# Optimization experiments

Measured on AMD Instinct MI355X. Metric: run time of the kernel, lower is better.

Reference implementation:

```python
import jax, jax.numpy as jnp
import numpy as np

DIM, HEADS = 1024, 16
HEAD_DIM = DIM // HEADS
SCALE = HEAD_DIM ** -0.5


def setup_inputs() -> dict:
    key = jax.random.key(0)
    ks = jax.random.split(key, 5)
    B, N = 2, 2048
    x = jax.random.normal(ks[0], (B, N, DIM), dtype=jnp.float32)
    freqs = jax.random.normal(ks[1], (N, HEAD_DIM // 2), dtype=jnp.float32)
    w_qkv = jax.random.normal(ks[2], (3 * DIM, DIM), dtype=jnp.float32) * 0.02
    w_proj = jax.random.normal(ks[3], (DIM, DIM), dtype=jnp.float32) * 0.02
    b_proj = jnp.zeros((DIM,), dtype=jnp.float32)
    return {"x": x, "freqs": freqs, "w_qkv": w_qkv, "w_proj": w_proj, "b_proj": b_proj}


def _apply_rotary(t, cos, sin):
    # t: (B,N,H,D); cos/sin: (1,N,1,D//2)
    B, N, H, D = t.shape
    tp = t.reshape(B, N, H, D // 2, 2)
    x1, x2 = tp[..., 0], tp[..., 1]
    out = jnp.stack([x1 * cos - x2 * sin, x1 * sin + x2 * cos], axis=-1)
    return out.reshape(B, N, H, D)


def reference(x, freqs, w_qkv, w_proj, b_proj):
    B, N, C = x.shape
    H, D = HEADS, HEAD_DIM
    qkv = (x @ w_qkv.T).reshape(B, N, 3, H, D)  # fused QKV projection
    q, k, v = qkv[:, :, 0], qkv[:, :, 1], qkv[:, :, 2]  # each (B,N,H,D)
    cos = jnp.cos(freqs)[None, :, None, :]  # (1,N,1,D/2)
    sin = jnp.sin(freqs)[None, :, None, :]
    q = _apply_rotary(q, cos, sin)
    k = _apply_rotary(k, cos, sin)
    # SDPA: scores (B,H,N,N)
    scores = jnp.einsum("bqhd,bkhd->bhqk", q, k) * SCALE
    attn = jax.nn.softmax(scores, axis=-1)
    out = jnp.einsum("bhqk,bkhd->bqhd", attn, v).reshape(B, N, C)
    return out @ w_proj.T + b_proj
```

## Files before the change

kernel.cpp:

```cpp
#include <hip/hip_runtime.h>
#include <hip/hip_bf16.h>
#include <stdint.h>

#define BATCH   2
#define SEQ     2048
#define CDIM    1024
#define NHEAD   16
#define HDIM    64
#define MROWS   (BATCH*SEQ)
#define QKVN    (3*CDIM)
#define ATT_SCALE 0.125f

typedef __hip_bfloat16 bf16;
using bf16x8 = __attribute__((ext_vector_type(8))) __bf16;
using f32x4  = __attribute__((ext_vector_type(4))) float;

__device__ __forceinline__ void gld16(const void* g, void* l) {
    __builtin_amdgcn_global_load_lds(
        (__attribute__((address_space(1))) void*)(void*)(g),
        (__attribute__((address_space(3))) void*)(l),
        16, 0, 0);
}

__device__ __forceinline__ f32x4 mfma16x16x32(bf16x8 a, bf16x8 b, f32x4 c) {
    return __builtin_amdgcn_mfma_f32_16x16x32_bf16(a, b, c, 0, 0, 0);
}

__device__ __forceinline__ void store_out(bf16* p, float v) { *p = __float2bfloat16(v); }
__device__ __forceinline__ void store_out(float* p, float v) { *p = v; }

__global__ __launch_bounds__(256)
void cvt_kernel(const float* __restrict__ x, const float* __restrict__ wq,
                const float* __restrict__ wp, bf16* __restrict__ xb,
                bf16* __restrict__ wqb, bf16* __restrict__ wpb) {
    const size_t NX = (size_t)MROWS*CDIM/4;
    const size_t NQ = (size_t)QKVN*CDIM/4;
    size_t i4 = (size_t)blockIdx.x*256 + threadIdx.x;
    const float* src; bf16* dst; size_t off;
    if (i4 < NX)           { src = x;  dst = xb;  off = i4; }
    else if (i4 < NX + NQ) { src = wq; dst = wqb; off = i4 - NX; }
    else                   { src = wp; dst = wpb; off = i4 - NX - NQ; }
    float4 v = ((const float4*)src)[off];
    bf16 o[4] = { __float2bfloat16(v.x), __float2bfloat16(v.y),
                  __float2bfloat16(v.z), __float2bfloat16(v.w) };
    *(uint64_t*)(dst + off*4) = *(const uint64_t*)o;
}

template<typename OutT, bool ADD_BIAS>
__global__ __launch_bounds__(256)
void gemm_bt(const bf16* __restrict__ A, const bf16* __restrict__ Bw,
             const float* __restrict__ bias, OutT* __restrict__ C,
             int M, int N, int K) {
    __shared__ __align__(16) bf16 As[128*32];
    __shared__ __align__(16) bf16 Bs[128*32];

    const int bm = blockIdx.x, bn = blockIdx.y;
    const int tid  = threadIdx.x;
    const int lane = tid & 63;
    const int w    = tid >> 6;
    const int wm   = (w & 1) * 64;
    const int wn   = (w >> 1) * 64;
    const int quad = lane >> 4;
    const int l16  = lane & 15;

    const int c0 = tid, c1 = tid + 256;
    const size_t a_off0 = (size_t)(bm*128 + (c0 >> 2)) * K + (c0 & 3) * 8;
    const size_t a_off1 = (size_t)(bm*128 + (c1 >> 2)) * K + (c1 & 3) * 8;
    const size_t b_off0 = (size_t)(bn*128 + (c0 >> 2)) * K + (c0 & 3) * 8;
    const size_t b_off1 = (size_t)(bn*128 + (c1 >> 2)) * K + (c1 & 3) * 8;

    f32x4 acc[4][4] = {};

    for (int k0 = 0; k0 < K; k0 += 32) {
        __syncthreads();
        gld16(A + a_off0 + k0, &As[c0*8]);
        gld16(A + a_off1 + k0, &As[c1*8]);
        gld16(Bw + b_off0 + k0, &Bs[c0*8]);
        gld16(Bw + b_off1 + k0, &Bs[c1*8]);
        __syncthreads();

        bf16x8 af[4], bfv[4];
#pragma unroll
        for (int i = 0; i < 4; i++)
            af[i] = *(const bf16x8*)&As[(wm + i*16 + l16)*32 + quad*8];
#pragma unroll
        for (int i = 0; i < 4; i++)
            bfv[i] = *(const bf16x8*)&Bs[(wn + i*16 + l16)*32 + quad*8];
#pragma unroll
        for (int mi = 0; mi < 4; mi++)
#pragma unroll
            for (int ni = 0; ni < 4; ni++)
                acc[mi][ni] = mfma16x16x32(af[mi], bfv[ni], acc[mi][ni]);
    }

#pragma unroll
    for (int mi = 0; mi < 4; mi++) {
        const int r0 = bm*128 + wm + mi*16 + quad*4;
#pragma unroll
        for (int ni = 0; ni < 4; ni++) {
            const int c = bn*128 + wn + ni*16 + l16;
            float bv = 0.f;
            if (ADD_BIAS) bv = bias[c];
#pragma unroll
            for (int r = 0; r < 4; r++)
                store_out(&C[(size_t)(r0 + r)*N + c], acc[mi][ni][r] + bv);
        }
    }
}

__global__ __launch_bounds__(256)
void rope_kernel(const bf16* __restrict__ qkv, const float* __restrict__ freqs,
                 bf16* __restrict__ Qr, bf16* __restrict__ Kr, bf16* __restrict__ VT) {
    const int blk = blockIdx.x;
    const int bh  = blk >> 5;
    const int b   = bh >> 4, h = bh & 15;
    const int n0  = (blk & 31) * 64;
    const int tid = threadIdx.x;

    __shared__ float cs[64][32];
    __shared__ float sn[64][32];
    __shared__ bf16  vt[64][65];

#pragma unroll
    for (int r = 0; r < 8; r++) {
        int idx = tid + 256*r;
        int nl = idx >> 5, i = idx & 31;
        float f = freqs[(size_t)(n0 + nl)*32 + i];
        cs[nl][i] = cosf(f);
        sn[nl][i] = sinf(f);
    }
    __syncthreads();

#pragma unroll
    for (int s = 0; s < 2; s++) {
        const bf16* src = qkv + s*CDIM;
        bf16* dst = (s == 0) ? Qr : Kr;
#pragma unroll
        for (int r = 0; r < 8; r++) {
            int idx = tid + 256*r;
            int nl = idx >> 5, i = idx & 31;
            const bf16* p = src + (size_t)(b*SEQ + n0 + nl)*QKVN + h*HDIM + 2*i;
            float x1 = __bfloat162float(p[0]);
            float x2 = __bfloat162float(p[1]);
            float c = cs[nl][i], sv = sn[nl][i];
            bf16* q = dst + ((size_t)bh*SEQ + n0 + nl)*HDIM + 2*i;
            q[0] = __float2bfloat16(x1*c - x2*sv);
            q[1] = __float2bfloat16(x1*sv + x2*c);
        }
    }

#pragma unroll
    for (int r = 0; r < 8; r++) {
        int idx = tid + 256*r;
        int nl = idx >> 5, dp = idx & 31;
        const bf16* p = qkv + (size_t)(b*SEQ + n0 + nl)*QKVN + 2*CDIM + h*HDIM + 2*dp;
        vt[nl][2*dp]   = p[0];
        vt[nl][2*dp+1] = p[1];
    }
    __syncthreads();
#pragma unroll
    for (int r = 0; r < 8; r++) {
        int idx = tid + 256*r;
        int d = idx >> 5, np = idx & 31;
        bf16* o = VT + ((size_t)bh*HDIM + d)*SEQ + n0 + 2*np;
        o[0] = vt[2*np][d];
        o[1] = vt[2*np+1][d];
    }
}

#define PSTRIDE 72

__global__ __launch_bounds__(256)
void attn_kernel(const bf16* __restrict__ Qr, const bf16* __restrict__ Kr,
                 const bf16* __restrict__ VT, bf16* __restrict__ Ao) {
    const int blk = blockIdx.x;
    const int bh  = blk >> 4;
    const int b   = bh >> 4, h = bh & 15;
    const int q0  = (blk & 15) * 128;
    const int tid = threadIdx.x;
    const int w   = tid >> 6, lane = tid & 63;
    const int quad = lane >> 4, l16 = lane & 15;

    __shared__ __align__(16) bf16 Ks[2][64*64];
    __shared__ __align__(16) bf16 Vs[2][64*64];
    __shared__ __align__(16) bf16 Ps[4][2*16*PSTRIDE];

    bf16x8 qf[2][2];
#pragma unroll
    for (int t = 0; t < 2; t++) {
        const int qrow = q0 + w*32 + t*16 + l16;
        const bf16* qp = Qr + ((size_t)bh*SEQ + qrow)*HDIM + quad*8;
        qf[t][0] = *(const bf16x8*)(qp);
        qf[t][1] = *(const bf16x8*)(qp + 32);
    }

    const int s0 = tid, s1 = tid + 256;
    const int r0 = s0 >> 3, g0 = (s0 & 7) ^ (r0 & 7);
    const int r1 = s1 >> 3, g1 = (s1 & 7) ^ (r1 & 7);
    const bf16* kb0 = Kr + (size_t)bh*SEQ*HDIM + r0*HDIM + g0*8;
    const bf16* kb1 = Kr + (size_t)bh*SEQ*HDIM + r1*HDIM + g1*8;
    const bf16* vb0 = VT + (size_t)bh*HDIM*SEQ + r0*SEQ + g0*8;
    const bf16* vb1 = VT + (size_t)bh*HDIM*SEQ + r1*SEQ + g1*8;

    f32x4 acc[2][4] = {};
    float lsum[2][4] = {};

    gld16(kb0, &Ks[0][s0*8]);
    gld16(kb1, &Ks[0][s1*8]);
    gld16(vb0, &Vs[0][s0*8]);
    gld16(vb1, &Vs[0][s1*8]);

    for (int it = 0; it < SEQ/64; ++it) {
        const int cur = it & 1, nxt = cur ^ 1;
        __syncthreads();
        if (it + 1 < SEQ/64) {
            const size_t ko = (size_t)(it + 1) * 64 * HDIM;
            const size_t vo = (size_t)(it + 1) * 64;
            gld16(kb0 + ko, &Ks[nxt][s0*8]);
            gld16(kb1 + ko, &Ks[nxt][s1*8]);
            gld16(vb0 + vo, &Vs[nxt][s0*8]);
            gld16(vb1 + vo, &Vs[nxt][s1*8]);
        }

        const int swz = (l16 & 7);
        f32x4 sv[2][4];
#pragma unroll
        for (int j = 0; j < 4; j++) {
            const bf16* krow = &Ks[cur][(j*16 + l16)*64];
            bf16x8 ka = *(const bf16x8*)(krow + ((quad     ^ swz) * 8));
            bf16x8 kb = *(const bf16x8*)(krow + (((quad+4) ^ swz) * 8));
#pragma unroll
            for (int t = 0; t < 2; t++) {
                f32x4 tacc = {};
                tacc = mfma16x16x32(qf[t][0], ka, tacc);
                tacc = mfma16x16x32(qf[t][1], kb, tacc);
                sv[t][j] = tacc;
            }
        }

#pragma unroll
        for (int t = 0; t < 2; t++) {
            bf16* pw = &Ps[w][t*16*PSTRIDE];
#pragma unroll
            for (int r = 0; r < 4; r++) {
                const int prow = (quad*4 + r) * PSTRIDE;
                float ls = 0.f;
#pragma unroll
                for (int j = 0; j < 4; j++) {
                    float e = __expf(sv[t][j][r] * ATT_SCALE);
                    ls += e;
                    pw[prow + j*16 + l16] = __float2bfloat16(e);
                }
                lsum[t][r] += ls;
            }
        }
        asm volatile("s_waitcnt lgkmcnt(0)" ::: "memory");

        bf16x8 pf[2][2];
#pragma unroll
        for (int t = 0; t < 2; t++) {
            const bf16* pr = &Ps[w][t*16*PSTRIDE + l16*PSTRIDE + quad*8];
            pf[t][0] = *(const bf16x8*)(pr);
            pf[t][1] = *(const bf16x8*)(pr + 32);
        }
#pragma unroll
        for (int dt = 0; dt < 4; dt++) {
            const bf16* vrow = &Vs[cur][(dt*16 + l16)*64];
            bf16x8 va = *(const bf16x8*)(vrow + ((quad     ^ swz) * 8));
            bf16x8 vb = *(const bf16x8*)(vrow + (((quad+4) ^ swz) * 8));
#pragma unroll
            for (int t = 0; t < 2; t++) {
                acc[t][dt] = mfma16x16x32(pf[t][0], va, acc[t][dt]);
                acc[t][dt] = mfma16x16x32(pf[t][1], vb, acc[t][dt]);
            }
        }
    }

#pragma unroll
    for (int t = 0; t < 2; t++)
#pragma unroll
        for (int r = 0; r < 4; r++) {
            float s_ = lsum[t][r];
#pragma unroll
            for (int off = 1; off < 16; off <<= 1)
                s_ += __shfl_xor(s_, off, 64);
            lsum[t][r] = s_;
        }

#pragma unroll
    for (int t = 0; t < 2; t++)
#pragma unroll
        for (int dt = 0; dt < 4; dt++)
#pragma unroll
            for (int r = 0; r < 4; r++) {
                int qr  = q0 + w*32 + t*16 + quad*4 + r;
                int col = h*HDIM + dt*16 + l16;
                Ao[(size_t)(b*SEQ + qr)*CDIM + col] =
                    __float2bfloat16(acc[t][dt][r] / lsum[t][r]);
            }
}

extern "C" void kernel_launch(void* const* d_in, const int* in_sizes, int n_in,
                              void* d_out, int out_size, void* d_ws, size_t ws_size,
                              hipStream_t stream) {
    const float* x      = (const float*)d_in[0];
    const float* freqs  = (const float*)d_in[1];
    const float* w_qkv  = (const float*)d_in[2];
    const float* w_proj = (const float*)d_in[3];
    const float* b_proj = (const float*)d_in[4];
    float* out = (float*)d_out;

    char* ws = (char*)d_ws;
    bf16* xb    = (bf16*)ws; ws += (size_t)MROWS * CDIM * sizeof(bf16);
    bf16* wqkvb = (bf16*)ws; ws += (size_t)QKVN * CDIM * sizeof(bf16);
    bf16* wprojb= (bf16*)ws; ws += (size_t)CDIM * CDIM * sizeof(bf16);
    bf16* qkv   = (bf16*)ws; ws += (size_t)MROWS * QKVN * sizeof(bf16);
    bf16* Qr    = (bf16*)ws; ws += (size_t)BATCH*NHEAD*SEQ*HDIM*sizeof(bf16);
    bf16* Kr    = (bf16*)ws; ws += (size_t)BATCH*NHEAD*SEQ*HDIM*sizeof(bf16);
    bf16* VT    = (bf16*)ws; ws += (size_t)BATCH*NHEAD*SEQ*HDIM*sizeof(bf16);
    bf16* Ao    = (bf16*)ws;

    dim3 blk(256);
    {
        size_t n4 = ((size_t)MROWS*CDIM + (size_t)QKVN*CDIM + (size_t)CDIM*CDIM) / 4;
        cvt_kernel<<<dim3((n4 + 255) / 256), blk, 0, stream>>>(
            x, w_qkv, w_proj, xb, wqkvb, wprojb);
    }
    gemm_bt<bf16, false><<<dim3(MROWS/128, QKVN/128), blk, 0, stream>>>(
        xb, wqkvb, nullptr, qkv, MROWS, QKVN, CDIM);
    rope_kernel<<<dim3(BATCH*NHEAD*(SEQ/64)), blk, 0, stream>>>(
        qkv, freqs, Qr, Kr, VT);
    attn_kernel<<<dim3(BATCH*NHEAD*(SEQ/128)), blk, 0, stream>>>(
        Qr, Kr, VT, Ao);
    gemm_bt<float, true><<<dim3(MROWS/128, CDIM/128), blk, 0, stream>>>(
        Ao, wprojb, b_proj, out, MROWS, CDIM, CDIM);
}
```

Measured before the change: 223.3 us.

## Fuse RoPE and V transpose into QKV GEMM epilogue, restructure softmax P stores

Removes the separate rope kernel and the intermediate qkv buffer: the QKV GEMM epilogue now applies rotary embedding to Q/K using shuffles between adjacent columns, and writes V transposed through shared memory. The cos/sin table is precomputed in the conversion kernel. In attention, the QK MFMA operands are swapped so each lane holds one query row's scores, which allows packed 64-bit P stores and a per-lane row sum with fewer shuffles. The trade-off is strided scalar stores for Q/K in the epilogue and extra shared-memory syncs in the V path.

```diff
diff --git a/kernel.cpp b/kernel.cpp
--- a/kernel.cpp
+++ b/kernel.cpp
@@ -26,33 +26,48 @@
     return __builtin_amdgcn_mfma_f32_16x16x32_bf16(a, b, c, 0, 0, 0);
 }
 
+__device__ __forceinline__ uint16_t bfbits(float v) {
+    bf16 b = __float2bfloat16(v);
+    return *(uint16_t*)&b;
+}
 __device__ __forceinline__ void store_out(bf16* p, float v) { *p = __float2bfloat16(v); }
 __device__ __forceinline__ void store_out(float* p, float v) { *p = v; }
 
+#define NX_F4 ((size_t)MROWS*CDIM/4)
+#define NQ_F4 ((size_t)QKVN*CDIM/4)
+#define NP_F4 ((size_t)CDIM*CDIM/4)
+#define NF_SC ((size_t)SEQ*32)
+
 __global__ __launch_bounds__(256)
 void cvt_kernel(const float* __restrict__ x, const float* __restrict__ wq,
-                const float* __restrict__ wp, bf16* __restrict__ xb,
-                bf16* __restrict__ wqb, bf16* __restrict__ wpb) {
-    const size_t NX = (size_t)MROWS*CDIM/4;
-    const size_t NQ = (size_t)QKVN*CDIM/4;
+                const float* __restrict__ wp, const float* __restrict__ freqs,
+                bf16* __restrict__ xb, bf16* __restrict__ wqb,
+                bf16* __restrict__ wpb, float2* __restrict__ csn) {
     size_t i4 = (size_t)blockIdx.x*256 + threadIdx.x;
-    const float* src; bf16* dst; size_t off;
-    if (i4 < NX)           { src = x;  dst = xb;  off = i4; }
-    else if (i4 < NX + NQ) { src = wq; dst = wqb; off = i4 - NX; }
-    else                   { src = wp; dst = wpb; off = i4 - NX - NQ; }
-    float4 v = ((const float4*)src)[off];
-    bf16 o[4] = { __float2bfloat16(v.x), __float2bfloat16(v.y),
-                  __float2bfloat16(v.z), __float2bfloat16(v.w) };
-    *(uint64_t*)(dst + off*4) = *(const uint64_t*)o;
-}
-
-template<typename OutT, bool ADD_BIAS>
+    if (i4 < NX_F4 + NQ_F4 + NP_F4) {
+        const float* src; bf16* dst; size_t off;
+        if (i4 < NX_F4)           { src = x;  dst = xb;  off = i4; }
+        else if (i4 < NX_F4+NQ_F4){ src = wq; dst = wqb; off = i4 - NX_F4; }
+        else                      { src = wp; dst = wpb; off = i4 - NX_F4 - NQ_F4; }
+        float4 v = ((const float4*)src)[off];
+        bf16 o[4] = { __float2bfloat16(v.x), __float2bfloat16(v.y),
+                      __float2bfloat16(v.z), __float2bfloat16(v.w) };
+        *(uint64_t*)(dst + off*4) = *(const uint64_t*)o;
+    } else if (i4 < NX_F4 + NQ_F4 + NP_F4 + NF_SC) {
+        size_t k = i4 - (NX_F4 + NQ_F4 + NP_F4);
+        float f = freqs[k];
+        csn[k] = make_float2(cosf(f), sinf(f));
+    }
+}
+
 __global__ __launch_bounds__(256)
-void gemm_bt(const bf16* __restrict__ A, const bf16* __restrict__ Bw,
-             const float* __restrict__ bias, OutT* __restrict__ C,
-             int M, int N, int K) {
-    __shared__ __align__(16) bf16 As[128*32];
-    __shared__ __align__(16) bf16 Bs[128*32];
+void gemm_qkv_rope(const bf16* __restrict__ A, const bf16* __restrict__ Bw,
+                   const float2* __restrict__ csn, bf16* __restrict__ Qr,
+                   bf16* __restrict__ Kr, bf16* __restrict__ VT) {
+    const int K = CDIM, N = QKVN;
+    __shared__ __align__(16) bf16 sh[64*136];
+    bf16* As = sh;
+    bf16* Bs = sh + 4096;
 
     const int bm = blockIdx.x, bn = blockIdx.y;
     const int tid  = threadIdx.x;
@@ -93,6 +108,108 @@
                 acc[mi][ni] = mfma16x16x32(af[mi], bfv[ni], acc[mi][ni]);
     }
 
+    const int region = bn >> 3;
+    if (region < 2) {
+        bf16* dst = region ? Kr : Qr;
+        const int odd = l16 & 1;
+#pragma unroll
+        for (int mi = 0; mi < 4; mi++) {
+#pragma unroll
+            for (int ni = 0; ni < 4; ni++) {
+                const int cq = (bn & 7)*128 + wn + ni*16 + l16;
+                const int h = cq >> 6, d = cq & 63, fi = d >> 1;
+#pragma unroll
+                for (int r = 0; r < 4; r++) {
+                    const int m = bm*128 + wm + mi*16 + quad*4 + r;
+                    const int bb = m >> 11, n = m & 2047;
+                    float own = acc[mi][ni][r];
+                    float prt = __shfl_xor(own, 1);
+                    float2 cs2 = csn[n*32 + fi];
+                    float o = odd ? (prt*cs2.y + own*cs2.x)
+                                  : (own*cs2.x - prt*cs2.y);
+                    dst[((size_t)(bb*16 + h)*SEQ + n)*HDIM + d] = __float2bfloat16(o);
+                }
+            }
+        }
+    } else {
+        const int bb = (bm*128) >> 11, n0 = (bm*128) & 2047;
+        __syncthreads();
+#pragma unroll
+        for (int cc = 0; cc < 2; ++cc) {
+            if ((w >> 1) == cc) {
+#pragma unroll
+                for (int mi = 0; mi < 4; mi++)
+#pragma unroll
+                    for (int ni = 0; ni < 4; ni++) {
+                        const int d  = ni*16 + l16;
+                        const int nl = wm + mi*16 + quad*4;
+                        uint2 pk;
+                        pk.x = (uint32_t)bfbits(acc[mi][ni][0]) |
+                               ((uint32_t)bfbits(acc[mi][ni][1]) << 16);
+                        pk.y = (uint32_t)bfbits(acc[mi][ni][2]) |
+                               ((uint32_t)bfbits(acc[mi][ni][3]) << 16);
+                        *(uint2*)&sh[d*136 + nl] = pk;
+                    }
+            }
+            __syncthreads();
+            const int h = (bn - 16)*2 + cc;
+            const int d = tid >> 2, tn = tid & 3;
+            bf16* vdst = VT + ((size_t)(bb*16 + h)*HDIM + d)*SEQ + n0 + tn*32;
+#pragma unroll
+            for (int j = 0; j < 4; j++)
+                *(uint4*)(vdst + j*8) = *(const uint4*)&sh[d*136 + tn*32 + j*8];
+            __syncthreads();
+        }
+    }
+}
+
+template<typename OutT, bool ADD_BIAS>
+__global__ __launch_bounds__(256)
+void gemm_bt(const bf16* __restrict__ A, const bf16* __restrict__ Bw,
+             const float* __restrict__ bias, OutT* __restrict__ C,
+             int M, int N, int K) {
+    __shared__ __align__(16) bf16 As[128*32];
+    __shared__ __align__(16) bf16 Bs[128*32];
+
+    const int bm = blockIdx.x, bn = blockIdx.y;
+    const int tid  = threadIdx.x;
+    const int lane = tid & 63;
+    const int w    = tid >> 6;
+    const int wm   = (w & 1) * 64;
+    const int wn   = (w >> 1) * 64;
+    const int quad = lane >> 4;
+    const int l16  = lane & 15;
+
+    const int c0 = tid, c1 = tid + 256;
+    const size_t a_off0 = (size_t)(bm*128 + (c0 >> 2)) * K + (c0 & 3) * 8;
+    const size_t a_off1 = (size_t)(bm*128 + (c1 >> 2)) * K + (c1 & 3) * 8;
+    const size_t b_off0 = (size_t)(bn*128 + (c0 >> 2)) * K + (c0 & 3) * 8;
+    const size_t b_off1 = (size_t)(bn*128 + (c1 >> 2)) * K + (c1 & 3) * 8;
+
+    f32x4 acc[4][4] = {};
+
+    for (int k0 = 0; k0 < K; k0 += 32) {
+        __syncthreads();
+        gld16(A + a_off0 + k0, &As[c0*8]);
+        gld16(A + a_off1 + k0, &As[c1*8]);
+        gld16(Bw + b_off0 + k0, &Bs[c0*8]);
+        gld16(Bw + b_off1 + k0, &Bs[c1*8]);
+        __syncthreads();
+
+        bf16x8 af[4], bfv[4];
+#pragma unroll
+        for (int i = 0; i < 4; i++)
+            af[i] = *(const bf16x8*)&As[(wm + i*16 + l16)*32 + quad*8];
+#pragma unroll
+        for (int i = 0; i < 4; i++)
+            bfv[i] = *(const bf16x8*)&Bs[(wn + i*16 + l16)*32 + quad*8];
+#pragma unroll
+        for (int mi = 0; mi < 4; mi++)
+#pragma unroll
+            for (int ni = 0; ni < 4; ni++)
+                acc[mi][ni] = mfma16x16x32(af[mi], bfv[ni], acc[mi][ni]);
+    }
+
 #pragma unroll
     for (int mi = 0; mi < 4; mi++) {
         const int r0 = bm*128 + wm + mi*16 + quad*4;
@@ -105,66 +222,6 @@
             for (int r = 0; r < 4; r++)
                 store_out(&C[(size_t)(r0 + r)*N + c], acc[mi][ni][r] + bv);
         }
-    }
-}
-
-__global__ __launch_bounds__(256)
-void rope_kernel(const bf16* __restrict__ qkv, const float* __restrict__ freqs,
-                 bf16* __restrict__ Qr, bf16* __restrict__ Kr, bf16* __restrict__ VT) {
-    const int blk = blockIdx.x;
-    const int bh  = blk >> 5;
-    const int b   = bh >> 4, h = bh & 15;
-    const int n0  = (blk & 31) * 64;
-    const int tid = threadIdx.x;
-
-    __shared__ float cs[64][32];
-    __shared__ float sn[64][32];
-    __shared__ bf16  vt[64][65];
-
-#pragma unroll
-    for (int r = 0; r < 8; r++) {
-        int idx = tid + 256*r;
-        int nl = idx >> 5, i = idx & 31;
-        float f = freqs[(size_t)(n0 + nl)*32 + i];
-        cs[nl][i] = cosf(f);
-        sn[nl][i] = sinf(f);
-    }
-    __syncthreads();
-
-#pragma unroll
-    for (int s = 0; s < 2; s++) {
-        const bf16* src = qkv + s*CDIM;
-        bf16* dst = (s == 0) ? Qr : Kr;
-#pragma unroll
-        for (int r = 0; r < 8; r++) {
-            int idx = tid + 256*r;
-            int nl = idx >> 5, i = idx & 31;
-            const bf16* p = src + (size_t)(b*SEQ + n0 + nl)*QKVN + h*HDIM + 2*i;
-            float x1 = __bfloat162float(p[0]);
-            float x2 = __bfloat162float(p[1]);
-            float c = cs[nl][i], sv = sn[nl][i];
-            bf16* q = dst + ((size_t)bh*SEQ + n0 + nl)*HDIM + 2*i;
-            q[0] = __float2bfloat16(x1*c - x2*sv);
-            q[1] = __float2bfloat16(x1*sv + x2*c);
-        }
-    }
-
-#pragma unroll
-    for (int r = 0; r < 8; r++) {
-        int idx = tid + 256*r;
-        int nl = idx >> 5, dp = idx & 31;
-        const bf16* p = qkv + (size_t)(b*SEQ + n0 + nl)*QKVN + 2*CDIM + h*HDIM + 2*dp;
-        vt[nl][2*dp]   = p[0];
-        vt[nl][2*dp+1] = p[1];
-    }
-    __syncthreads();
-#pragma unroll
-    for (int r = 0; r < 8; r++) {
-        int idx = tid + 256*r;
-        int d = idx >> 5, np = idx & 31;
-        bf16* o = VT + ((size_t)bh*HDIM + d)*SEQ + n0 + 2*np;
-        o[0] = vt[2*np][d];
-        o[1] = vt[2*np+1][d];
     }
 }
 
@@ -203,12 +260,14 @@
     const bf16* vb1 = VT + (size_t)bh*HDIM*SEQ + r1*SEQ + g1*8;
 
     f32x4 acc[2][4] = {};
-    float lsum[2][4] = {};
+    float lsum[2] = {0.f, 0.f};
 
     gld16(kb0, &Ks[0][s0*8]);
     gld16(kb1, &Ks[0][s1*8]);
     gld16(vb0, &Vs[0][s0*8]);
     gld16(vb1, &Vs[0][s1*8]);
+
+    const int swz = l16 & 7;
 
     for (int it = 0; it < SEQ/64; ++it) {
         const int cur = it & 1, nxt = cur ^ 1;
@@ -222,7 +281,6 @@
             gld16(vb1 + vo, &Vs[nxt][s1*8]);
         }
 
-        const int swz = (l16 & 7);
         f32x4 sv[2][4];
 #pragma unroll
         for (int j = 0; j < 4; j++) {
@@ -232,26 +290,25 @@
 #pragma unroll
             for (int t = 0; t < 2; t++) {
                 f32x4 tacc = {};
-                tacc = mfma16x16x32(qf[t][0], ka, tacc);
-                tacc = mfma16x16x32(qf[t][1], kb, tacc);
+                tacc = mfma16x16x32(ka, qf[t][0], tacc);
+                tacc = mfma16x16x32(kb, qf[t][1], tacc);
                 sv[t][j] = tacc;
             }
         }
 
 #pragma unroll
         for (int t = 0; t < 2; t++) {
-            bf16* pw = &Ps[w][t*16*PSTRIDE];
-#pragma unroll
-            for (int r = 0; r < 4; r++) {
-                const int prow = (quad*4 + r) * PSTRIDE;
-                float ls = 0.f;
-#pragma unroll
-                for (int j = 0; j < 4; j++) {
-                    float e = __expf(sv[t][j][r] * ATT_SCALE);
-                    ls += e;
-                    pw[prow + j*16 + l16] = __float2bfloat16(e);
-                }
-                lsum[t][r] += ls;
+#pragma unroll
+            for (int j = 0; j < 4; j++) {
+                float e0 = __expf(sv[t][j][0] * ATT_SCALE);
+                float e1 = __expf(sv[t][j][1] * ATT_SCALE);
+                float e2 = __expf(sv[t][j][2] * ATT_SCALE);
+                float e3 = __expf(sv[t][j][3] * ATT_SCALE);
+                lsum[t] += (e0 + e1) + (e2 + e3);
+                uint2 pk;
+                pk.x = (uint32_t)bfbits(e0) | ((uint32_t)bfbits(e1) << 16);
+                pk.y = (uint32_t)bfbits(e2) | ((uint32_t)bfbits(e3) << 16);
+                *(uint2*)&Ps[w][(t*16 + l16)*PSTRIDE + j*16 + quad*4] = pk;
             }
         }
         asm volatile("s_waitcnt lgkmcnt(0)" ::: "memory");
@@ -259,7 +316,7 @@
         bf16x8 pf[2][2];
 #pragma unroll
         for (int t = 0; t < 2; t++) {
-            const bf16* pr = &Ps[w][t*16*PSTRIDE + l16*PSTRIDE + quad*8];
+            const bf16* pr = &Ps[w][(t*16 + l16)*PSTRIDE + quad*8];
             pf[t][0] = *(const bf16x8*)(pr);
             pf[t][1] = *(const bf16x8*)(pr + 32);
         }
@@ -277,15 +334,16 @@
     }
 
 #pragma unroll
+    for (int t = 0; t < 2; t++) {
+        lsum[t] += __shfl_xor(lsum[t], 16, 64);
+        lsum[t] += __shfl_xor(lsum[t], 32, 64);
+    }
+    float lt[2][4];
+#pragma unroll
     for (int t = 0; t < 2; t++)
 #pragma unroll
-        for (int r = 0; r < 4; r++) {
-            float s_ = lsum[t][r];
-#pragma unroll
-            for (int off = 1; off < 16; off <<= 1)
-                s_ += __shfl_xor(s_, off, 64);
-            lsum[t][r] = s_;
-        }
+        for (int r = 0; r < 4; r++)
+            lt[t][r] = __shfl(lsum[t], quad*20 + r, 64);
 
 #pragma unroll
     for (int t = 0; t < 2; t++)
@@ -296,7 +354,7 @@
                 int qr  = q0 + w*32 + t*16 + quad*4 + r;
                 int col = h*HDIM + dt*16 + l16;
                 Ao[(size_t)(b*SEQ + qr)*CDIM + col] =
-                    __float2bfloat16(acc[t][dt][r] / lsum[t][r]);
+                    __float2bfloat16(acc[t][dt][r] / lt[t][r]);
             }
 }
 
@@ -311,25 +369,23 @@
     float* out = (float*)d_out;
 
     char* ws = (char*)d_ws;
-    bf16* xb    = (bf16*)ws; ws += (size_t)MROWS * CDIM * sizeof(bf16);
-    bf16* wqkvb = (bf16*)ws; ws += (size_t)QKVN * CDIM * sizeof(bf16);
-    bf16* wprojb= (bf16*)ws; ws += (size_t)CDIM * CDIM * sizeof(bf16);
-    bf16* qkv   = (bf16*)ws; ws += (size_t)MROWS * QKVN * sizeof(bf16);
-    bf16* Qr    = (bf16*)ws; ws += (size_t)BATCH*NHEAD*SEQ*HDIM*sizeof(bf16);
-    bf16* Kr    = (bf16*)ws; ws += (size_t)BATCH*NHEAD*SEQ*HDIM*sizeof(bf16);
-    bf16* VT    = (bf16*)ws; ws += (size_t)BATCH*NHEAD*SEQ*HDIM*sizeof(bf16);
-    bf16* Ao    = (bf16*)ws;
+    bf16*   xb    = (bf16*)ws;   ws += (size_t)MROWS * CDIM * sizeof(bf16);
+    bf16*   wqkvb = (bf16*)ws;   ws += (size_t)QKVN * CDIM * sizeof(bf16);
+    bf16*   wprojb= (bf16*)ws;   ws += (size_t)CDIM * CDIM * sizeof(bf16);
+    float2* csn   = (float2*)ws; ws += (size_t)SEQ * 32 * sizeof(float2);
+    bf16*   Qr    = (bf16*)ws;   ws += (size_t)BATCH*NHEAD*SEQ*HDIM*sizeof(bf16);
+    bf16*   Kr    = (bf16*)ws;   ws += (size_t)BATCH*NHEAD*SEQ*HDIM*sizeof(bf16);
+    bf16*   VT    = (bf16*)ws;   ws += (size_t)BATCH*NHEAD*SEQ*HDIM*sizeof(bf16);
+    bf16*   Ao    = (bf16*)ws;
 
     dim3 blk(256);
     {
-        size_t n4 = ((size_t)MROWS*CDIM + (size_t)QKVN*CDIM + (size_t)CDIM*CDIM) / 4;
-        cvt_kernel<<<dim3((n4 + 255) / 256), blk, 0, stream>>>(
-            x, w_qkv, w_proj, xb, wqkvb, wprojb);
-    }
-    gemm_bt<bf16, false><<<dim3(MROWS/128, QKVN/128), blk, 0, stream>>>(
-        xb, wqkvb, nullptr, qkv, MROWS, QKVN, CDIM);
-    rope_kernel<<<dim3(BATCH*NHEAD*(SEQ/64)), blk, 0, stream>>>(
-        qkv, freqs, Qr, Kr, VT);
+        size_t nthr = NX_F4 + NQ_F4 + NP_F4 + NF_SC;
+        cvt_kernel<<<dim3((nthr + 255) / 256), blk, 0, stream>>>(
+            x, w_qkv, w_proj, freqs, xb, wqkvb, wprojb, csn);
+    }
+    gemm_qkv_rope<<<dim3(MROWS/128, QKVN/128), blk, 0, stream>>>(
+        xb, wqkvb, csn, Qr, Kr, VT);
     attn_kernel<<<dim3(BATCH*NHEAD*(SEQ/128)), blk, 0, stream>>>(
         Qr, Kr, VT, Ao);
     gemm_bt<float, true><<<dim3(MROWS/128, CDIM/128), blk, 0, stream>>>(
```

Measured after the change: 221.5 us. About the same (-0.8%).
